# Kernel tuning notes

Measured on AMD Instinct MI355X. Metric: run time of the kernel, lower is better.

## Reference

```python
import jax, jax.numpy as jnp
import numpy as np

GROUPSIZE = 128

def _unpack_int4(packed, axis):
    # packed: int32 array; unpack 8 nibbles per int32 along `axis`.
    shifts = (jnp.arange(8, dtype=jnp.int32) * 4)
    expanded = jnp.expand_dims(packed, axis + 1)  # [..., P, 1, ...]
    shp = [1] * expanded.ndim
    shp[axis + 1] = 8
    nib = (expanded >> shifts.reshape(shp)) & 0xF
    new_shape = list(packed.shape)
    new_shape[axis] = packed.shape[axis] * 8
    return nib.reshape(new_shape)

def setup_inputs() -> dict:
    key = jax.random.key(0)
    k1, k2, k3, k4, k5 = jax.random.split(key, 5)
    in_f, out_f = 4096, 4096
    n_tokens = 8192
    n_groups = in_f // GROUPSIZE
    x = jax.random.normal(k1, (n_tokens, in_f), dtype=jnp.float32)
    qweight = jax.random.randint(k2, (in_f // 8, out_f), 0, 2147483647, dtype=jnp.int32)
    qzeros = jax.random.randint(k3, (n_groups, out_f // 8), 0, 2147483647, dtype=jnp.int32)
    scales = jax.random.uniform(k4, (n_groups, out_f), dtype=jnp.float32) * 0.01
    g_idx = (jnp.arange(in_f, dtype=jnp.int32) // GROUPSIZE).astype(jnp.int32)
    bias = jax.random.normal(k5, (out_f,), dtype=jnp.float32) * 0.01
    return {"x": x, "qweight": qweight, "qzeros": qzeros,
            "scales": scales, "g_idx": g_idx, "bias": bias}

def reference(x, qweight, qzeros, scales, g_idx, bias):
    # Dequantize int4 GPTQ weights: W[k,n] = scales[g_idx[k],n] * (wq[k,n] - (zq[g_idx[k],n]+1))
    wq = _unpack_int4(qweight, axis=0)          # [in, out] int32 nibbles
    zq = _unpack_int4(qzeros, axis=1) + 1       # [n_groups, out]
    scale_k = scales[g_idx]                     # [in, out]
    zero_k = zq[g_idx]                          # [in, out]
    w = scale_k * (wq.astype(x.dtype) - zero_k.astype(x.dtype))  # [in, out]
    return x @ w + bias
```

## Files before the change

### kernel.cpp

```cpp
#include <hip/hip_runtime.h>

typedef __attribute__((ext_vector_type(4))) float  f32x4;
typedef __attribute__((ext_vector_type(8))) short  short8;
typedef __attribute__((ext_vector_type(4))) short  short4v;

#define M_TOK 8192
#define N_OUT 4096
#define K_IN  4096
#define NT    64

typedef const __attribute__((address_space(1))) void* gp_t;
typedef __attribute__((address_space(3))) void* lp_t;
__device__ __forceinline__ void gl_lds16(const void* g, void* l) {
    __builtin_amdgcn_global_load_lds((gp_t)g, (lp_t)l, 16, 0, 0);
}

#define CVT_BLOCKS 16384

__global__ __launch_bounds__(256)
void prep(const float* __restrict__ x, unsigned short* __restrict__ xb,
          const int* __restrict__ qweight, const int* __restrict__ qzeros,
          const float* __restrict__ scales, unsigned short* __restrict__ Wt) {
    __shared__ unsigned short wt[64][80];
    const int t = threadIdx.x;

    if (blockIdx.x < CVT_BLOCKS) {
        const size_t i = ((size_t)blockIdx.x * 256 + t) * 8;
        f32x4 a = *(const f32x4*)(x + i);
        f32x4 b = *(const f32x4*)(x + i + 4);
        union { short8 v; __bf16 h[8]; } u;
        u.h[0] = (__bf16)a.x; u.h[1] = (__bf16)a.y; u.h[2] = (__bf16)a.z; u.h[3] = (__bf16)a.w;
        u.h[4] = (__bf16)b.x; u.h[5] = (__bf16)b.y; u.h[6] = (__bf16)b.z; u.h[7] = (__bf16)b.w;
        *(short8*)(xb + i) = u.v;
        return;
    }

    const int db = blockIdx.x - CVT_BLOCKS;
    const int k0 = (db & 63) * 64;
    const int n0 = (db >> 6) * 64;
    const int n  = t & 63;
    const int pl = t >> 6;
    const int g  = k0 >> 7;
    const int ncol = n0 + n;

    const float scale = scales[g * N_OUT + ncol];
    const int qz  = qzeros[g * (N_OUT / 8) + (ncol >> 3)];
    const int zp1 = ((qz >> ((ncol & 7) * 4)) & 0xF) + 1;
    const float zs = -(float)zp1 * scale;

    const int p0 = k0 >> 3;
    #pragma unroll
    for (int i = 0; i < 2; ++i) {
        const int p_local = pl + i * 4;
        const int q = qweight[(size_t)(p0 + p_local) * N_OUT + ncol];
        union { short8 v; __bf16 h[8]; } u;
        #pragma unroll
        for (int j = 0; j < 8; ++j)
            u.h[j] = (__bf16)fmaf((float)((q >> (4 * j)) & 0xF), scale, zs);
        *(short8*)(&wt[n][8 * p_local]) = u.v;
    }
    __syncthreads();

    #pragma unroll
    for (int it = 0; it < 2; ++it) {
        const int row   = (t >> 3) + 32 * it;
        const int chunk = t & 7;
        short8 v = *(const short8*)(&wt[row][chunk * 8]);
        *(short8*)(Wt + (size_t)(n0 + row) * K_IN + k0 + chunk * 8) = v;
    }
}

__global__ __launch_bounds__(512, 2)
void gemm_bf16_ph(const unsigned short* __restrict__ xb,
                  const unsigned short* __restrict__ Wt,
                  const float* __restrict__ bias,
                  float* __restrict__ out)
{
    const int tid  = threadIdx.x;
    const int lane = tid & 63;
    const int wid  = tid >> 6;
    const int wm   = wid >> 2;
    const int wn   = wid & 3;

    const int bid = blockIdx.x;
    const int swz = (bid & 7) * 64 + (bid >> 3);
    const int m0 = (swz >> 4) * 256;
    const int n0 = (swz & 15) * 256;

    __shared__ __align__(16) unsigned char lds[131072];
    unsigned char* Ab = lds;
    unsigned char* Bb = lds + 65536;

    f32x4 acc[8][4];
    #pragma unroll
    for (int i = 0; i < 8; ++i)
        #pragma unroll
        for (int j = 0; j < 4; ++j)
            acc[i][j] = f32x4{0.f, 0.f, 0.f, 0.f};

    const int sw8    = ((tid & 7) ^ ((tid >> 3) & 7)) * 8;
    const int a_srow = tid >> 3;
    const int b_srow = (wid >> 2) * 64 + (wid & 3) * 8 + (lane >> 3);
    const int a_dst  = wid * 1024;
    const int b_dst  = (wid >> 2) * 8192 + (wid & 3) * 1024;

    const int col0 = (((lane >> 4))     ^ (lane & 7)) << 4;
    const int col1 = ((4 | (lane >> 4)) ^ (lane & 7)) << 4;
    const int arow = (wm * 128 + (lane & 15)) * 128;
    const int brow = (wn * 64  + (lane & 15)) * 128;

    short8 af[4][2], b0[2][2], b1[2][2];

#define CFENCE asm volatile("" ::: "memory")

#define STAGE_A(SEL, KT, H) do { \
    _Pragma("unroll") for (int j_ = 0; j_ < 2; ++j_) \
        gl_lds16(xb + (size_t)(m0 + j_ * 128 + (H) * 64 + a_srow) * K_IN + (KT) * 64 + sw8, \
                 Ab + (SEL) * 32768 + j_ * 16384 + (H) * 8192 + a_dst); } while (0)

#define STAGE_B(SEL, KT, H) do { \
    _Pragma("unroll") for (int j_ = 0; j_ < 2; ++j_) \
        gl_lds16(Wt + (size_t)(n0 + j_ * 128 + (H) * 32 + b_srow) * K_IN + (KT) * 64 + sw8, \
                 Bb + (SEL) * 32768 + j_ * 16384 + (H) * 4096 + b_dst); } while (0)

#define LOAD_A(SEL, HM) do { \
    _Pragma("unroll") for (int mi_ = 0; mi_ < 4; ++mi_) { \
        af[mi_][0] = *(const short8*)(Ab + (SEL) * 32768 + arow + (HM) * 8192 + mi_ * 2048 + col0); \
        af[mi_][1] = *(const short8*)(Ab + (SEL) * 32768 + arow + (HM) * 8192 + mi_ * 2048 + col1); } } while (0)

#define LOAD_B(DST, SEL, HN) do { \
    _Pragma("unroll") for (int ni_ = 0; ni_ < 2; ++ni_) { \
        DST[ni_][0] = *(const short8*)(Bb + (SEL) * 32768 + brow + (HN) * 4096 + ni_ * 2048 + col0); \
        DST[ni_][1] = *(const short8*)(Bb + (SEL) * 32768 + brow + (HN) * 4096 + ni_ * 2048 + col1); } } while (0)

#define MFMA_Q(HM, HN, BF) do { \
    _Pragma("unroll") for (int mi_ = 0; mi_ < 4; ++mi_) \
    _Pragma("unroll") for (int ni_ = 0; ni_ < 2; ++ni_) \
    _Pragma("unroll") for (int kk_ = 0; kk_ < 2; ++kk_) \
        acc[(HM) * 4 + mi_][(HN) * 2 + ni_] = __builtin_amdgcn_mfma_f32_16x16x32_bf16( \
            af[mi_][kk_], BF[ni_][kk_], acc[(HM) * 4 + mi_][(HN) * 2 + ni_], 0, 0, 0); } while (0)

#define K_STEP(CUR, NXT) do { \
     \
    LOAD_A(CUR, 0); \
    LOAD_B(b0, CUR, 0); \
    CFENCE; \
    STAGE_A(NXT, ktn, 0); \
    STAGE_B(NXT, ktn, 0); \
    asm volatile("s_waitcnt vmcnt(6)" ::: "memory"); \
    __builtin_amdgcn_s_barrier(); \
    asm volatile("s_waitcnt lgkmcnt(0)" ::: "memory"); \
    __builtin_amdgcn_sched_barrier(0); \
    __builtin_amdgcn_s_setprio(1); \
    MFMA_Q(0, 0, b0); \
    __builtin_amdgcn_s_setprio(0); \
     \
    LOAD_B(b1, CUR, 1); \
    CFENCE; \
    STAGE_B(NXT, ktn, 1); \
    asm volatile("s_waitcnt vmcnt(6)" ::: "memory"); \
    __builtin_amdgcn_s_barrier(); \
    asm volatile("s_waitcnt lgkmcnt(0)" ::: "memory"); \
    __builtin_amdgcn_sched_barrier(0); \
    __builtin_amdgcn_s_setprio(1); \
    MFMA_Q(0, 1, b1); \
    __builtin_amdgcn_s_setprio(0); \
     \
    LOAD_A(CUR, 1); \
    CFENCE; \
    STAGE_A(NXT, ktn, 1); \
    __builtin_amdgcn_s_barrier(); \
    asm volatile("s_waitcnt lgkmcnt(0)" ::: "memory"); \
    __builtin_amdgcn_sched_barrier(0); \
    __builtin_amdgcn_s_setprio(1); \
    MFMA_Q(1, 0, b0); \
    __builtin_amdgcn_s_setprio(0); \
     \
    asm volatile("s_waitcnt vmcnt(4)" ::: "memory"); \
    __builtin_amdgcn_s_barrier(); \
    __builtin_amdgcn_sched_barrier(0); \
    __builtin_amdgcn_s_setprio(1); \
    MFMA_Q(1, 1, b1); \
    __builtin_amdgcn_s_setprio(0); \
} while (0)

    STAGE_A(0, 0, 0);
    CFENCE;
    STAGE_B(0, 0, 0);
    CFENCE;
    STAGE_B(0, 0, 1);
    CFENCE;
    STAGE_A(0, 0, 1);
    asm volatile("s_waitcnt vmcnt(4)" ::: "memory");
    __builtin_amdgcn_s_barrier();

    int ktn;
    #pragma unroll 1
    for (int kt = 0; kt < NT; kt += 2) {
        ktn = kt + 1;
        K_STEP(0, 1);
        ktn = (kt + 2) & (NT - 1);
        K_STEP(1, 0);
    }

#undef STAGE_A
#undef STAGE_B
#undef LOAD_A
#undef LOAD_B
#undef MFMA_Q
#undef K_STEP
#undef CFENCE

    const int col_base = n0 + wn * 64 + (lane & 15);
    const int row_base = m0 + wm * 128 + (lane >> 4) * 4;
    #pragma unroll
    for (int fn = 0; fn < 4; ++fn) {
        const int col = col_base + fn * 16;
        const float bv = bias[col];
        #pragma unroll
        for (int fm = 0; fm < 8; ++fm) {
            #pragma unroll
            for (int r = 0; r < 4; ++r) {
                const int row = row_base + fm * 16 + r;
                out[(size_t)row * N_OUT + col] = acc[fm][fn][r] + bv;
            }
        }
    }
}

__global__ __launch_bounds__(256, 2)
void gptq_gemm_fused(const float* __restrict__ x,
                     const int*   __restrict__ qweight,
                     const int*   __restrict__ qzeros,
                     const float* __restrict__ scales,
                     const float* __restrict__ bias,
                     float*       __restrict__ out)
{
    const int tid  = threadIdx.x;
    const int lane = tid & 63;
    const int wid  = tid >> 6;
    const int wm   = wid >> 1;
    const int wn   = wid & 1;
    const int m0 = blockIdx.y * 128;
    const int n0 = blockIdx.x * 128;

    __shared__ __align__(16) unsigned char lds[32768];
    unsigned char* Ab = lds;
    unsigned char* Bb = lds + 16384;

    const int ar  = tid >> 4;
    const int ac4 = (tid & 15) * 4;
    const int bnn = tid & 127;
    const int bph = tid >> 7;
    const int ncol = n0 + bnn;

    f32x4 a_reg[8];
    int   q_reg[4];
    float scale_r = 0.f, zs_r = 0.f;

    f32x4 acc[4][4];
    #pragma unroll
    for (int i = 0; i < 4; ++i)
        #pragma unroll
        for (int j = 0; j < 4; ++j)
            acc[i][j] = f32x4{0.f, 0.f, 0.f, 0.f};

    auto load_tile = [&](int kt) {
        const int k0 = kt * 64;
        #pragma unroll
        for (int i = 0; i < 8; ++i)
            a_reg[i] = *(const f32x4*)(x + (size_t)(m0 + ar + 16 * i) * K_IN + k0 + ac4);
        const int p0 = k0 >> 3;
        #pragma unroll
        for (int i = 0; i < 4; ++i)
            q_reg[i] = qweight[(size_t)(p0 + i * 2 + bph) * N_OUT + ncol];
        const int g = k0 >> 7;
        scale_r = scales[g * N_OUT + ncol];
        const int qz = qzeros[g * (N_OUT / 8) + (ncol >> 3)];
        zs_r = -(float)(((qz >> ((ncol & 7) * 4)) & 0xF) + 1) * scale_r;
    };

    auto store_tile = [&]() {
        #pragma unroll
        for (int i = 0; i < 8; ++i) {
            const int r = ar + 16 * i;
            const int addr = r * 128 + ((ac4 * 2) ^ ((r & 7) << 4));
            union { short4v v; __bf16 h[4]; } u;
            u.h[0] = (__bf16)a_reg[i].x; u.h[1] = (__bf16)a_reg[i].y;
            u.h[2] = (__bf16)a_reg[i].z; u.h[3] = (__bf16)a_reg[i].w;
            *(short4v*)(Ab + addr) = u.v;
        }
        #pragma unroll
        for (int i = 0; i < 4; ++i) {
            const int pl = i * 2 + bph;
            const int q  = q_reg[i];
            union { short8 v; __bf16 h[8]; } u;
            #pragma unroll
            for (int j = 0; j < 8; ++j)
                u.h[j] = (__bf16)fmaf((float)((q >> (4 * j)) & 0xF), scale_r, zs_r);
            const int addr = bnn * 128 + ((pl * 16) ^ ((bnn & 7) << 4));
            *(short8*)(Bb + addr) = u.v;
        }
    };

    auto compute_tile = [&]() {
        #pragma unroll
        for (int kk = 0; kk < 2; ++kk) {
            short8 afr[4], bfr[4];
            const int cb = kk * 64 + (lane >> 4) * 16;
            #pragma unroll
            for (int mi = 0; mi < 4; ++mi) {
                const int r = wm * 64 + mi * 16 + (lane & 15);
                afr[mi] = *(const short8*)(Ab + r * 128 + (cb ^ ((r & 7) << 4)));
            }
            #pragma unroll
            for (int ni = 0; ni < 4; ++ni) {
                const int nn = wn * 64 + ni * 16 + (lane & 15);
                bfr[ni] = *(const short8*)(Bb + nn * 128 + (cb ^ ((nn & 7) << 4)));
            }
            #pragma unroll
            for (int mi = 0; mi < 4; ++mi)
                #pragma unroll
                for (int ni = 0; ni < 4; ++ni)
                    acc[mi][ni] = __builtin_amdgcn_mfma_f32_16x16x32_bf16(
                        afr[mi], bfr[ni], acc[mi][ni], 0, 0, 0);
        }
    };

    load_tile(0);
    for (int kt = 0; kt < 64; ++kt) {
        if (kt) __syncthreads();
        store_tile();
        __syncthreads();
        if (kt + 1 < 64) load_tile(kt + 1);
        compute_tile();
    }

    const int col_base = n0 + wn * 64 + (lane & 15);
    const int row_base = m0 + wm * 64 + (lane >> 4) * 4;
    #pragma unroll
    for (int ni = 0; ni < 4; ++ni) {
        const int col = col_base + ni * 16;
        const float bv = bias[col];
        #pragma unroll
        for (int mi = 0; mi < 4; ++mi)
            #pragma unroll
            for (int r = 0; r < 4; ++r)
                out[(size_t)(row_base + mi * 16 + r) * N_OUT + col] = acc[mi][ni][r] + bv;
    }
}

extern "C" void kernel_launch(void* const* d_in, const int* in_sizes, int n_in,
                              void* d_out, int out_size, void* d_ws, size_t ws_size,
                              hipStream_t stream) {
    const float* x       = (const float*)d_in[0];
    const int*   qweight = (const int*)  d_in[1];
    const int*   qzeros  = (const int*)  d_in[2];
    const float* scales  = (const float*)d_in[3];
    const float* bias    = (const float*)d_in[5];
    float* out = (float*)d_out;

    const size_t xb_bytes = (size_t)M_TOK * K_IN * 2;
    const size_t wt_bytes = (size_t)N_OUT * K_IN * 2;

    if (ws_size >= xb_bytes + wt_bytes) {
        unsigned short* xb = (unsigned short*)d_ws;
        unsigned short* Wt = (unsigned short*)((char*)d_ws + xb_bytes);
        prep<<<dim3(CVT_BLOCKS + (K_IN / 64) * (N_OUT / 64)), dim3(256), 0, stream>>>(
            x, xb, qweight, qzeros, scales, Wt);
        gemm_bf16_ph<<<dim3((M_TOK / 256) * (N_OUT / 256)), dim3(512), 0, stream>>>(xb, Wt, bias, out);
    } else {
        gptq_gemm_fused<<<dim3(N_OUT / 128, M_TOK / 128), dim3(256), 0, stream>>>(
            x, qweight, qzeros, scales, bias, out);
    }
}
```

Measured before the change: 257.4 us.

## Deepen GEMM prefetch to two tiles ahead, refilling the consumed buffer in place

Reworks the double-buffered GEMM main loop so each k-step refills the same LDS buffer it just consumed with the tile two steps ahead, after barriers confirm that buffer's halves have been read. The prologue now stages both buffers, and each global load has roughly a full extra k-step to land. The goal is to hide more global-memory latency behind the MFMA work. In exchange there are more barriers per step and waitcnt accounting that is harder to get right, so an off-by-one could cause stalls or LDS races.

```diff
diff --git a/kernel.cpp b/kernel.cpp
--- a/kernel.cpp
+++ b/kernel.cpp
@@ -71,10 +71,10 @@
 }
 
 __global__ __launch_bounds__(512, 2)
-void gemm_bf16_ph(const unsigned short* __restrict__ xb,
-                  const unsigned short* __restrict__ Wt,
-                  const float* __restrict__ bias,
-                  float* __restrict__ out)
+void gemm_bf16_dpr(const unsigned short* __restrict__ xb,
+                   const unsigned short* __restrict__ Wt,
+                   const float* __restrict__ bias,
+                   float* __restrict__ out)
 {
     const int tid  = threadIdx.x;
     const int lane = tid & 63;
@@ -140,14 +140,10 @@
         acc[(HM) * 4 + mi_][(HN) * 2 + ni_] = __builtin_amdgcn_mfma_f32_16x16x32_bf16( \
             af[mi_][kk_], BF[ni_][kk_], acc[(HM) * 4 + mi_][(HN) * 2 + ni_], 0, 0, 0); } while (0)
 
-#define K_STEP(CUR, NXT) do { \
+#define K_STEP(CUR) do { \
      \
     LOAD_A(CUR, 0); \
     LOAD_B(b0, CUR, 0); \
-    CFENCE; \
-    STAGE_A(NXT, ktn, 0); \
-    STAGE_B(NXT, ktn, 0); \
-    asm volatile("s_waitcnt vmcnt(6)" ::: "memory"); \
     __builtin_amdgcn_s_barrier(); \
     asm volatile("s_waitcnt lgkmcnt(0)" ::: "memory"); \
     __builtin_amdgcn_sched_barrier(0); \
@@ -156,10 +152,10 @@
     __builtin_amdgcn_s_setprio(0); \
      \
     LOAD_B(b1, CUR, 1); \
+    __builtin_amdgcn_s_barrier(); \
     CFENCE; \
-    STAGE_B(NXT, ktn, 1); \
-    asm volatile("s_waitcnt vmcnt(6)" ::: "memory"); \
-    __builtin_amdgcn_s_barrier(); \
+    STAGE_A(CUR, ktn2, 0); \
+    STAGE_B(CUR, ktn2, 0); \
     asm volatile("s_waitcnt lgkmcnt(0)" ::: "memory"); \
     __builtin_amdgcn_sched_barrier(0); \
     __builtin_amdgcn_s_setprio(1); \
@@ -167,17 +163,19 @@
     __builtin_amdgcn_s_setprio(0); \
      \
     LOAD_A(CUR, 1); \
+    __builtin_amdgcn_s_barrier(); \
     CFENCE; \
-    STAGE_A(NXT, ktn, 1); \
-    __builtin_amdgcn_s_barrier(); \
+    STAGE_B(CUR, ktn2, 1); \
     asm volatile("s_waitcnt lgkmcnt(0)" ::: "memory"); \
     __builtin_amdgcn_sched_barrier(0); \
     __builtin_amdgcn_s_setprio(1); \
     MFMA_Q(1, 0, b0); \
     __builtin_amdgcn_s_setprio(0); \
      \
-    asm volatile("s_waitcnt vmcnt(4)" ::: "memory"); \
+    asm volatile("s_waitcnt vmcnt(6)" ::: "memory"); \
     __builtin_amdgcn_s_barrier(); \
+    CFENCE; \
+    STAGE_A(CUR, ktn2, 1); \
     __builtin_amdgcn_sched_barrier(0); \
     __builtin_amdgcn_s_setprio(1); \
     MFMA_Q(1, 1, b1); \
@@ -191,16 +189,24 @@
     STAGE_B(0, 0, 1);
     CFENCE;
     STAGE_A(0, 0, 1);
-    asm volatile("s_waitcnt vmcnt(4)" ::: "memory");
+    CFENCE;
+    STAGE_A(1, 1, 0);
+    CFENCE;
+    STAGE_B(1, 1, 0);
+    CFENCE;
+    STAGE_B(1, 1, 1);
+    CFENCE;
+    STAGE_A(1, 1, 1);
+    asm volatile("s_waitcnt vmcnt(8)" ::: "memory");
     __builtin_amdgcn_s_barrier();
 
-    int ktn;
+    int ktn2;
     #pragma unroll 1
     for (int kt = 0; kt < NT; kt += 2) {
-        ktn = kt + 1;
-        K_STEP(0, 1);
-        ktn = (kt + 2) & (NT - 1);
-        K_STEP(1, 0);
+        ktn2 = (kt + 2) & (NT - 1);
+        K_STEP(0);
+        ktn2 = (kt + 3) & (NT - 1);
+        K_STEP(1);
     }
 
 #undef STAGE_A
@@ -368,7 +374,7 @@
         unsigned short* Wt = (unsigned short*)((char*)d_ws + xb_bytes);
         prep<<<dim3(CVT_BLOCKS + (K_IN / 64) * (N_OUT / 64)), dim3(256), 0, stream>>>(
             x, xb, qweight, qzeros, scales, Wt);
-        gemm_bf16_ph<<<dim3((M_TOK / 256) * (N_OUT / 256)), dim3(512), 0, stream>>>(xb, Wt, bias, out);
+        gemm_bf16_dpr<<<dim3((M_TOK / 256) * (N_OUT / 256)), dim3(512), 0, stream>>>(xb, Wt, bias, out);
     } else {
         gptq_gemm_fused<<<dim3(N_OUT / 128, M_TOK / 128), dim3(256), 0, stream>>>(
             x, qweight, qzeros, scales, bias, out);
```

Measured after the change: 257.9 us. No clear change (+0.2%).
